# Kernel optimization log

Hardware: AMD Instinct MI355X
Metric: run time of the kernel (lower is better)

Reference implementation:

```python
import jax, jax.numpy as jnp
import numpy as np

B, T, S, E, H, L, V = 32, 64, 64, 512, 1024, 2, 32000


def setup_inputs() -> dict:
    key = jax.random.key(0)
    ks = jax.random.split(key, 20)
    std = 0.02
    inp = {
        "x": jax.random.randint(ks[0], (B, T), 0, V),
        "h0": jax.random.normal(ks[1], (L, B, H), jnp.float32) * std,
        "c0": jax.random.normal(ks[2], (L, B, H), jnp.float32) * std,
        "x_enc": jax.random.normal(ks[3], (B, S, H), jnp.float32),
        "emb": jax.random.normal(ks[4], (V, E), jnp.float32) * std,
        # layer 0: input = concat(emb, prev_out) -> E + H
        "Wih0": jax.random.normal(ks[5], (4 * H, E + H), jnp.float32) * std,
        "Whh0": jax.random.normal(ks[6], (4 * H, H), jnp.float32) * std,
        "bih0": jnp.zeros((4 * H,), jnp.float32),
        "bhh0": jnp.zeros((4 * H,), jnp.float32),
        # layer 1: input = h of layer 0 -> H
        "Wih1": jax.random.normal(ks[7], (4 * H, H), jnp.float32) * std,
        "Whh1": jax.random.normal(ks[8], (4 * H, H), jnp.float32) * std,
        "bih1": jnp.zeros((4 * H,), jnp.float32),
        "bhh1": jnp.zeros((4 * H,), jnp.float32),
        # attention linear H->H
        "Wa": jax.random.normal(ks[9], (H, H), jnp.float32) * std,
        "ba": jnp.zeros((H,), jnp.float32),
        # output linear 2H->H
        "Wl": jax.random.normal(ks[10], (H, 2 * H), jnp.float32) * std,
        "bl": jnp.zeros((H,), jnp.float32),
        # generator H->V
        "Wg": jax.random.normal(ks[11], (V, H), jnp.float32) * std,
        "bg": jnp.zeros((V,), jnp.float32),
    }
    return inp


def _decoder_fwd(x, h0, c0, x_enc, emb, Wih0, Whh0, bih0, bhh0,
                 Wih1, Whh1, bih1, bhh1, Wa, ba, Wl, bl, Wg, bg):
    layers = ((Wih0, Whh0, bih0, bhh0), (Wih1, Whh1, bih1, bhh1))
    xs = emb[x]  # [B, T, E]

    def lstm_cell(inp, h_prev, c_prev, Wih, Whh, bih, bhh):
        g = inp @ Wih.T + bih + h_prev @ Whh.T + bhh  # [B, 4H]
        i_, f_, g_, o_ = jnp.split(g, 4, axis=-1)     # torch order: i,f,g,o
        c_new = jax.nn.sigmoid(f_) * c_prev + jax.nn.sigmoid(i_) * jnp.tanh(g_)
        h_new = jax.nn.sigmoid(o_) * jnp.tanh(c_new)
        return h_new, c_new

    def step(carry, e_t):
        h, c, prev = carry  # h,c: [L,B,H]; prev: [B,H]
        inp = jnp.concatenate([e_t, prev], axis=-1)  # [B, E+H]
        hs, cs = [], []
        for l, (Wih, Whh, bih, bhh) in enumerate(layers):
            h_new, c_new = lstm_cell(inp, h[l], c[l], Wih, Whh, bih, bhh)
            hs.append(h_new); cs.append(c_new)
            inp = h_new
        z = inp  # top-layer hidden [B, H]
        # attention: score = linear(z) . x_enc^T
        s = jnp.einsum('bh,bsh->bs', z @ Wa.T + ba, x_enc)  # [B, S]
        w = jax.nn.softmax(s, axis=-1)
        ctx = jnp.einsum('bs,bsh->bh', w, x_enc)            # [B, H]
        out = jnp.tanh(jnp.concatenate([z, ctx], axis=-1) @ Wl.T + bl)  # [B, H]
        return (jnp.stack(hs), jnp.stack(cs), out), out

    prev0 = jnp.zeros((x.shape[0], Wl.shape[0]), xs.dtype)
    e_seq = jnp.swapaxes(xs[:, :-1, :], 0, 1)  # [T-1, B, E]
    _, outs = jax.lax.scan(step, (h0, c0, prev0), e_seq)
    outs = jnp.swapaxes(outs, 0, 1)  # [B, T-1, H]
    # dropout p=0.0 (eval) -> identity; generator: linear + log_softmax
    return jax.nn.log_softmax(outs @ Wg.T + bg, axis=-1)  # [B, T-1, V]


def reference(x, h0, c0, x_enc, emb, Wih0, Whh0, bih0, bhh0,
              Wih1, Whh1, bih1, bhh1, Wa, ba, Wl, bl, Wg, bg):
    return _decoder_fwd(x, h0, c0, x_enc, emb, Wih0, Whh0, bih0, bhh0,
                        Wih1, Whh1, bih1, bhh1, Wa, ba, Wl, bl, Wg, bg)
```

## Files before the change

kernel.cpp:

```cpp
#include <hip/hip_runtime.h>
#include <math.h>

#define BB 32
#define HH 1024
#define EE 512
#define TT 63
#define SS 64
#define VV 32000

__global__ __launch_bounds__(256)
void init_kernel(const float* __restrict__ h0, const float* __restrict__ c0,
                 float* __restrict__ h_state, float* __restrict__ c_state,
                 float* __restrict__ prev0)
{
    int i = blockIdx.x * 256 + threadIdx.x;
    if (i < 2 * BB * HH) { h_state[i] = h0[i]; c_state[i] = c0[i]; }
    if (i < BB * HH) prev0[i] = 0.f;
}

__global__ __launch_bounds__(128)
void embed_kernel(const int* __restrict__ x, const float* __restrict__ emb,
                  float* __restrict__ xs)
{
    int t = blockIdx.x >> 5;
    int b = blockIdx.x & 31;
    int tok = x[b * 64 + t];
    const float4* src = (const float4*)(emb + (size_t)tok * EE);
    float4* dst = (float4*)(xs + ((size_t)t * BB + b) * EE);
    dst[threadIdx.x] = src[threadIdx.x];
}

__global__ __launch_bounds__(256)
void lstm_step_kernel(const float* __restrict__ src0, int K0,
                      const float* __restrict__ src1, int K1,
                      const float* __restrict__ Wih, const float* __restrict__ Whh,
                      const float* __restrict__ bih, const float* __restrict__ bhh,
                      const float* __restrict__ h_prev, const float* __restrict__ c_prev,
                      float* __restrict__ h_new, float* __restrict__ c_new)
{
    __shared__ float lds[64 * 33];
    const int tid  = threadIdx.x;
    const int b    = tid & 31;
    const int hl   = tid >> 5;
    const int h    = blockIdx.x * 8 + hl;
    const int lane = tid & 63;
    const int wv   = tid >> 6;
    const int KW   = K0 + K1;
    const int Ktot = KW + HH;

    float acc0 = 0.f, acc1 = 0.f, acc2 = 0.f, acc3 = 0.f;

    for (int k0 = 0; k0 < Ktot; k0 += 64) {
        const float* s; int koff; int stride;
        if (k0 < K0)      { s = src0;   koff = k0;        stride = K0; }
        else if (k0 < KW) { s = src1;   koff = k0 - K0;   stride = K1; }
        else              { s = h_prev; koff = k0 - KW;   stride = HH; }
        #pragma unroll
        for (int r = 0; r < 8; ++r) {
            int bb = wv * 8 + r;
            lds[lane * 33 + bb] = s[(size_t)bb * stride + koff + lane];
        }
        __syncthreads();

        const float *wi, *wf, *wg, *wo;
        if (k0 < KW) {
            wi = Wih + (size_t)h            * KW + k0;
            wf = Wih + (size_t)(HH   + h)   * KW + k0;
            wg = Wih + (size_t)(2*HH + h)   * KW + k0;
            wo = Wih + (size_t)(3*HH + h)   * KW + k0;
        } else {
            int c = k0 - KW;
            wi = Whh + (size_t)h            * HH + c;
            wf = Whh + (size_t)(HH   + h)   * HH + c;
            wg = Whh + (size_t)(2*HH + h)   * HH + c;
            wo = Whh + (size_t)(3*HH + h)   * HH + c;
        }
        #pragma unroll
        for (int k = 0; k < 64; k += 4) {
            float4 vi = *(const float4*)(wi + k);
            float4 vf = *(const float4*)(wf + k);
            float4 vg = *(const float4*)(wg + k);
            float4 vo = *(const float4*)(wo + k);
            float x0 = lds[(k+0)*33 + b];
            float x1 = lds[(k+1)*33 + b];
            float x2 = lds[(k+2)*33 + b];
            float x3 = lds[(k+3)*33 + b];
            acc0 = fmaf(x0, vi.x, acc0); acc0 = fmaf(x1, vi.y, acc0);
            acc0 = fmaf(x2, vi.z, acc0); acc0 = fmaf(x3, vi.w, acc0);
            acc1 = fmaf(x0, vf.x, acc1); acc1 = fmaf(x1, vf.y, acc1);
            acc1 = fmaf(x2, vf.z, acc1); acc1 = fmaf(x3, vf.w, acc1);
            acc2 = fmaf(x0, vg.x, acc2); acc2 = fmaf(x1, vg.y, acc2);
            acc2 = fmaf(x2, vg.z, acc2); acc2 = fmaf(x3, vg.w, acc2);
            acc3 = fmaf(x0, vo.x, acc3); acc3 = fmaf(x1, vo.y, acc3);
            acc3 = fmaf(x2, vo.z, acc3); acc3 = fmaf(x3, vo.w, acc3);
        }
        __syncthreads();
    }

    float gi = acc0 + bih[h]        + bhh[h];
    float gf = acc1 + bih[HH + h]   + bhh[HH + h];
    float gg = acc2 + bih[2*HH + h] + bhh[2*HH + h];
    float go = acc3 + bih[3*HH + h] + bhh[3*HH + h];
    float si = 1.f / (1.f + expf(-gi));
    float sf = 1.f / (1.f + expf(-gf));
    float so = 1.f / (1.f + expf(-go));
    float cp = c_prev[(size_t)b * HH + h];
    float cn = sf * cp + si * tanhf(gg);
    float hn = so * tanhf(cn);
    h_new[(size_t)b * HH + h] = hn;
    c_new[(size_t)b * HH + h] = cn;
}

__global__ __launch_bounds__(256)
void linear_kernel(const float* __restrict__ src0, int K0,
                   const float* __restrict__ src1, int K1,
                   const float* __restrict__ W, const float* __restrict__ bias,
                   float* __restrict__ out, int N, int act)
{
    __shared__ float lds[64 * 33];
    const int tid  = threadIdx.x;
    const int b    = tid & 31;
    const int nl   = tid >> 5;
    const int n    = blockIdx.x * 8 + nl;
    const int lane = tid & 63;
    const int wv   = tid >> 6;
    const int K    = K0 + K1;
    float acc = 0.f;
    const float* wr = W + (size_t)n * K;
    for (int k0 = 0; k0 < K; k0 += 64) {
        const float* s; int koff; int stride;
        if (k0 < K0) { s = src0; koff = k0;      stride = K0; }
        else         { s = src1; koff = k0 - K0; stride = K1; }
        #pragma unroll
        for (int r = 0; r < 8; ++r) {
            int bb = wv * 8 + r;
            lds[lane * 33 + bb] = s[(size_t)bb * stride + koff + lane];
        }
        __syncthreads();
        #pragma unroll
        for (int k = 0; k < 64; k += 4) {
            float4 w4 = *(const float4*)(wr + k0 + k);
            acc = fmaf(lds[(k+0)*33 + b], w4.x, acc);
            acc = fmaf(lds[(k+1)*33 + b], w4.y, acc);
            acc = fmaf(lds[(k+2)*33 + b], w4.z, acc);
            acc = fmaf(lds[(k+3)*33 + b], w4.w, acc);
        }
        __syncthreads();
    }
    float r = acc + bias[n];
    if (act) r = tanhf(r);
    out[(size_t)b * N + n] = r;
}

__global__ __launch_bounds__(256)
void attn_kernel(const float* __restrict__ za, const float* __restrict__ x_enc,
                 float* __restrict__ ctx)
{
    __shared__ float zs[HH];
    __shared__ float pp[256];
    __shared__ float wgt[SS];
    const int tid = threadIdx.x;
    const int b = blockIdx.x;
    for (int i = tid; i < HH; i += 256) zs[i] = za[(size_t)b * HH + i];
    __syncthreads();
    int j = tid >> 2, part = tid & 3;
    const float* xe = x_enc + ((size_t)b * SS + j) * HH + part * 256;
    const float* zp = zs + part * 256;
    float p = 0.f;
    for (int k = 0; k < 256; ++k) p = fmaf(zp[k], xe[k], p);
    pp[tid] = p;
    __syncthreads();
    if (tid < SS) {
        float sc = pp[tid*4] + pp[tid*4+1] + pp[tid*4+2] + pp[tid*4+3];
        float m = sc;
        for (int off = 32; off; off >>= 1) m = fmaxf(m, __shfl_xor(m, off));
        float e = expf(sc - m);
        float ssum = e;
        for (int off = 32; off; off >>= 1) ssum += __shfl_xor(ssum, off);
        wgt[tid] = e / ssum;
    }
    __syncthreads();
    for (int k = tid; k < HH; k += 256) {
        float a = 0.f;
        const float* xb = x_enc + (size_t)b * SS * HH + k;
        #pragma unroll 8
        for (int jj = 0; jj < SS; ++jj) a = fmaf(wgt[jj], xb[(size_t)jj * HH], a);
        ctx[(size_t)b * HH + k] = a;
    }
}

__global__ __launch_bounds__(256)
void gen_gemm_kernel(const float* __restrict__ outs, const float* __restrict__ Wg,
                     const float* __restrict__ bg, float* __restrict__ out)
{
    __shared__ float As[32 * 68];
    __shared__ float Bs[64 * 68];
    const int tid = threadIdx.x;
    const int tn = tid & 15, tm = tid >> 4;
    const int vbase = blockIdx.x * 64;
    const int rbase = blockIdx.y * 32;
    float acc[2][4] = {};

    const int arow = tid >> 3;
    const int acol = (tid & 7) * 8;
    int rg = rbase + arow;
    int ab = rg / TT, at = rg % TT;
    const float* asrc = outs + ((size_t)at * BB + ab) * HH + acol;
    const int brow = tid >> 2;
    const int bcol = (tid & 3) * 16;
    const float* bsrc = Wg + (size_t)(vbase + brow) * HH + bcol;

    for (int k0 = 0; k0 < HH; k0 += 64) {
        float4 a4a = *(const float4*)(asrc + k0);
        float4 a4b = *(const float4*)(asrc + k0 + 4);
        *(float4*)&As[arow*68 + acol]     = a4a;
        *(float4*)&As[arow*68 + acol + 4] = a4b;
        float4 q0 = *(const float4*)(bsrc + k0);
        float4 q1 = *(const float4*)(bsrc + k0 + 4);
        float4 q2 = *(const float4*)(bsrc + k0 + 8);
        float4 q3 = *(const float4*)(bsrc + k0 + 12);
        *(float4*)&Bs[brow*68 + bcol]      = q0;
        *(float4*)&Bs[brow*68 + bcol + 4]  = q1;
        *(float4*)&Bs[brow*68 + bcol + 8]  = q2;
        *(float4*)&Bs[brow*68 + bcol + 12] = q3;
        __syncthreads();
        #pragma unroll
        for (int k = 0; k < 64; k += 4) {
            float4 a0 = *(const float4*)&As[(tm*2+0)*68 + k];
            float4 a1 = *(const float4*)&As[(tm*2+1)*68 + k];
            float4 b0 = *(const float4*)&Bs[(tn*4+0)*68 + k];
            float4 b1 = *(const float4*)&Bs[(tn*4+1)*68 + k];
            float4 b2 = *(const float4*)&Bs[(tn*4+2)*68 + k];
            float4 b3 = *(const float4*)&Bs[(tn*4+3)*68 + k];
            acc[0][0] += a0.x*b0.x + a0.y*b0.y + a0.z*b0.z + a0.w*b0.w;
            acc[0][1] += a0.x*b1.x + a0.y*b1.y + a0.z*b1.z + a0.w*b1.w;
            acc[0][2] += a0.x*b2.x + a0.y*b2.y + a0.z*b2.z + a0.w*b2.w;
            acc[0][3] += a0.x*b3.x + a0.y*b3.y + a0.z*b3.z + a0.w*b3.w;
            acc[1][0] += a1.x*b0.x + a1.y*b0.y + a1.z*b0.z + a1.w*b0.w;
            acc[1][1] += a1.x*b1.x + a1.y*b1.y + a1.z*b1.z + a1.w*b1.w;
            acc[1][2] += a1.x*b2.x + a1.y*b2.y + a1.z*b2.z + a1.w*b2.w;
            acc[1][3] += a1.x*b3.x + a1.y*b3.y + a1.z*b3.z + a1.w*b3.w;
        }
        __syncthreads();
    }
    #pragma unroll
    for (int i = 0; i < 2; ++i) {
        int r = rbase + tm*2 + i;
        #pragma unroll
        for (int jj = 0; jj < 4; ++jj) {
            int v = vbase + tn*4 + jj;
            out[(size_t)r * VV + v] = acc[i][jj] + bg[v];
        }
    }
}

__global__ __launch_bounds__(256)
void logsoftmax_kernel(float* __restrict__ out)
{
    __shared__ float red[4];
    __shared__ float red2[4];
    const int tid = threadIdx.x;
    float* row = out + (size_t)blockIdx.x * VV;
    float m = -1e30f;
    for (int i = tid; i < VV; i += 256) m = fmaxf(m, row[i]);
    for (int off = 32; off; off >>= 1) m = fmaxf(m, __shfl_xor(m, off));
    if ((tid & 63) == 0) red[tid >> 6] = m;
    __syncthreads();
    m = fmaxf(fmaxf(red[0], red[1]), fmaxf(red[2], red[3]));
    float s = 0.f;
    for (int i = tid; i < VV; i += 256) s += expf(row[i] - m);
    for (int off = 32; off; off >>= 1) s += __shfl_xor(s, off);
    if ((tid & 63) == 0) red2[tid >> 6] = s;
    __syncthreads();
    s = red2[0] + red2[1] + red2[2] + red2[3];
    float lse = m + logf(s);
    for (int i = tid; i < VV; i += 256) row[i] = row[i] - lse;
}

extern "C" void kernel_launch(void* const* d_in, const int* in_sizes, int n_in,
                              void* d_out, int out_size, void* d_ws, size_t ws_size,
                              hipStream_t stream)
{
    (void)in_sizes; (void)n_in; (void)out_size; (void)ws_size;
    const int*   x    = (const int*)  d_in[0];
    const float* h0   = (const float*)d_in[1];
    const float* c0   = (const float*)d_in[2];
    const float* x_enc= (const float*)d_in[3];
    const float* emb  = (const float*)d_in[4];
    const float* Wih0 = (const float*)d_in[5];
    const float* Whh0 = (const float*)d_in[6];
    const float* bih0 = (const float*)d_in[7];
    const float* bhh0 = (const float*)d_in[8];
    const float* Wih1 = (const float*)d_in[9];
    const float* Whh1 = (const float*)d_in[10];
    const float* bih1 = (const float*)d_in[11];
    const float* bhh1 = (const float*)d_in[12];
    const float* Wa   = (const float*)d_in[13];
    const float* ba   = (const float*)d_in[14];
    const float* Wl   = (const float*)d_in[15];
    const float* bl   = (const float*)d_in[16];
    const float* Wg   = (const float*)d_in[17];
    const float* bg   = (const float*)d_in[18];
    float* out = (float*)d_out;

    float* ws      = (float*)d_ws;
    float* h_state = ws;
    float* c_state = h_state + 131072;
    float* prev0   = c_state + 131072;
    float* za      = prev0   + 32768;
    float* ctx     = za      + 32768;
    float* xs      = ctx     + 32768;
    float* outs    = xs      + (size_t)TT * BB * EE;

    init_kernel<<<256, 256, 0, stream>>>(h0, c0, h_state, c_state, prev0);
    embed_kernel<<<TT * BB, 128, 0, stream>>>(x, emb, xs);

    for (int t = 0; t < TT; ++t) {
        const float* e_t  = xs + (size_t)t * BB * EE;
        const float* prev = (t == 0) ? prev0 : (outs + (size_t)(t - 1) * BB * HH);
        float* hc = h_state + (size_t)(t & 1) * 65536;
        float* hn = h_state + (size_t)((t + 1) & 1) * 65536;
        float* cc = c_state + (size_t)(t & 1) * 65536;
        float* cn = c_state + (size_t)((t + 1) & 1) * 65536;
        lstm_step_kernel<<<128, 256, 0, stream>>>(e_t, EE, prev, HH,
            Wih0, Whh0, bih0, bhh0, hc, cc, hn, cn);
        lstm_step_kernel<<<128, 256, 0, stream>>>(hn, HH, nullptr, 0,
            Wih1, Whh1, bih1, bhh1, hc + 32768, cc + 32768, hn + 32768, cn + 32768);
        linear_kernel<<<128, 256, 0, stream>>>(hn + 32768, HH, nullptr, 0,
            Wa, ba, za, HH, 0);
        attn_kernel<<<BB, 256, 0, stream>>>(za, x_enc, ctx);
        linear_kernel<<<128, 256, 0, stream>>>(hn + 32768, HH, ctx, HH,
            Wl, bl, outs + (size_t)t * BB * HH, HH, 1);
    }

    gen_gemm_kernel<<<dim3(VV / 64, 2016 / 32), 256, 0, stream>>>(outs, Wg, bg, out);
    logsoftmax_kernel<<<2016, 256, 0, stream>>>(out);
}
```

Measured before the change: 28.03 ms.

## Run decoder loop as persistent cooperative kernel with transposed weights and split-K GEMMs

Replaces the per-timestep launches with one cooperative persistent kernel that steps through all timesteps using grid-wide syncs. Weights are pre-transposed into the output buffer used as scratch, and the gate GEMMs are split over K into partial sums that a finalize phase reduces. The attention projection is moved off the recurrence by precomputing Wa applied to x_enc plus a bias term. The aim is to remove launch overhead and raise parallelism in the small-batch GEMVs, at the cost of grid-sync latency, extra partial-sum traffic and reliance on cooperative-launch support.

```diff
diff --git a/kernel.cpp b/kernel.cpp
--- a/kernel.cpp
+++ b/kernel.cpp
@@ -1,5 +1,8 @@
 #include <hip/hip_runtime.h>
+#include <hip/hip_cooperative_groups.h>
 #include <math.h>
+
+namespace cg = cooperative_groups;
 
 #define BB 32
 #define HH 1024
@@ -8,185 +11,316 @@
 #define SS 64
 #define VV 32000
 
-__global__ __launch_bounds__(256)
-void init_kernel(const float* __restrict__ h0, const float* __restrict__ c0,
-                 float* __restrict__ h_state, float* __restrict__ c_state,
-                 float* __restrict__ prev0)
+static const size_t OWT0 = 0;
+static const size_t OWT1 = 10485760;
+static const size_t OWLT = 18874368;
+static const size_t OXC0 = 20971520;
+static const size_t OXC1 = 26214400;
+static const size_t OGP  = 30408704;
+static const size_t OOP  = 34603008;
+static const size_t OPE  = 35651584;
+static const size_t OCB  = 37748736;
+
+__device__ __forceinline__ void fma4(float4& a, float s, const float4 w) {
+    a.x = fmaf(s, w.x, a.x);
+    a.y = fmaf(s, w.y, a.y);
+    a.z = fmaf(s, w.z, a.z);
+    a.w = fmaf(s, w.w, a.w);
+}
+
+template<int WPITCH, int NRT>
+__device__ __forceinline__ void pgemm(const float* __restrict__ W,
+                                      const float* __restrict__ X, int xpitch,
+                                      int kslice, float* __restrict__ P)
+{
+    const int tid = threadIdx.x, lane = tid & 63, wv = tid >> 6;
+    const int nU = NRT * 32;
+    for (int u = blockIdx.x; u < nU; u += gridDim.x) {
+        const int rt = u >> 5, kg = u & 31;
+        const int r0 = rt * 256 + lane * 4;
+        const int b0 = wv * 8;
+        const int kbase = kg * kslice;
+        const float* wb = W + (size_t)kbase * WPITCH + r0;
+        const float* xb = X + (size_t)b0 * xpitch + kbase;
+        float4 acc[8];
+        #pragma unroll
+        for (int i = 0; i < 8; ++i) acc[i] = make_float4(0.f, 0.f, 0.f, 0.f);
+        #pragma unroll 2
+        for (int kk = 0; kk < kslice; kk += 4) {
+            float4 w0 = *(const float4*)(wb + (size_t)(kk + 0) * WPITCH);
+            float4 w1 = *(const float4*)(wb + (size_t)(kk + 1) * WPITCH);
+            float4 w2 = *(const float4*)(wb + (size_t)(kk + 2) * WPITCH);
+            float4 w3 = *(const float4*)(wb + (size_t)(kk + 3) * WPITCH);
+            #pragma unroll
+            for (int i = 0; i < 8; ++i) {
+                float4 xv = *(const float4*)(xb + (size_t)i * xpitch + kk);
+                fma4(acc[i], xv.x, w0);
+                fma4(acc[i], xv.y, w1);
+                fma4(acc[i], xv.z, w2);
+                fma4(acc[i], xv.w, w3);
+            }
+        }
+        float* pp = P + ((size_t)kg * BB + b0) * WPITCH + r0;
+        #pragma unroll
+        for (int i = 0; i < 8; ++i) *(float4*)(pp + (size_t)i * WPITCH) = acc[i];
+    }
+}
+
+__device__ __forceinline__ void lstm_fin(const float* __restrict__ P,
+    const float* __restrict__ bih, const float* __restrict__ bhh,
+    float* __restrict__ cst,
+    float* __restrict__ hA, int pA, int oA,
+    float* __restrict__ hB, int pB, int oB,
+    float* __restrict__ smem)
+{
+    const int tid = threadIdx.x, lane = tid & 63, g = tid >> 6;
+    for (int u = blockIdx.x; u < 512; u += gridDim.x) {
+        const int b = u >> 4, hc = u & 15;
+        const int h = hc * 64 + lane;
+        float s = 0.f;
+        #pragma unroll
+        for (int sl = 0; sl < 32; ++sl)
+            s += P[((size_t)sl * BB + b) * 4096 + g * 1024 + h];
+        s += bih[g * 1024 + h] + bhh[g * 1024 + h];
+        smem[g * 64 + lane] = s;
+        __syncthreads();
+        if (tid < 64) {
+            float gi = smem[lane], gf = smem[64 + lane];
+            float gg = smem[128 + lane], go = smem[192 + lane];
+            float si = 1.f / (1.f + expf(-gi));
+            float sf = 1.f / (1.f + expf(-gf));
+            float so = 1.f / (1.f + expf(-go));
+            float cp = cst[(size_t)b * 1024 + h];
+            float cn = sf * cp + si * tanhf(gg);
+            float hn = so * tanhf(cn);
+            cst[(size_t)b * 1024 + h] = cn;
+            hA[(size_t)b * pA + oA + h] = hn;
+            hB[(size_t)b * pB + oB + h] = hn;
+        }
+        __syncthreads();
+    }
+}
+
+__device__ __forceinline__ void attn_phase(const float* __restrict__ xenc,
+    const float* __restrict__ pe, const float* __restrict__ cb,
+    float* __restrict__ zc, float* __restrict__ smem)
+{
+    const int tid = threadIdx.x;
+    float* zl = smem;
+    float* pp = smem + 1024;
+    float* wt = smem + 1280;
+    for (int u = blockIdx.x; u < 32; u += gridDim.x) {
+        const int b = u;
+        for (int i = tid; i < 1024; i += 256) zl[i] = zc[(size_t)b * 2048 + i];
+        __syncthreads();
+        {
+            const int j = tid >> 2, part = tid & 3;
+            const float* per = pe + ((size_t)b * 64 + j) * 1024 + part * 256;
+            const float* zp = zl + part * 256;
+            float p0 = 0.f, p1 = 0.f, p2 = 0.f, p3 = 0.f;
+            for (int k = 0; k < 256; k += 4) {
+                p0 = fmaf(zp[k], per[k], p0);
+                p1 = fmaf(zp[k + 1], per[k + 1], p1);
+                p2 = fmaf(zp[k + 2], per[k + 2], p2);
+                p3 = fmaf(zp[k + 3], per[k + 3], p3);
+            }
+            pp[tid] = (p0 + p1) + (p2 + p3);
+        }
+        __syncthreads();
+        if (tid < 64) {
+            float sc = pp[tid * 4] + pp[tid * 4 + 1] + pp[tid * 4 + 2] + pp[tid * 4 + 3]
+                     + cb[b * 64 + tid];
+            float m = sc;
+            #pragma unroll
+            for (int off = 32; off; off >>= 1) m = fmaxf(m, __shfl_xor(m, off));
+            float e = expf(sc - m);
+            float ss = e;
+            #pragma unroll
+            for (int off = 32; off; off >>= 1) ss += __shfl_xor(ss, off);
+            wt[tid] = e / ss;
+        }
+        __syncthreads();
+        for (int k = tid; k < 1024; k += 256) {
+            float a = 0.f;
+            const float* xe = xenc + (size_t)b * (SS * HH) + k;
+            #pragma unroll 8
+            for (int j = 0; j < SS; ++j) a = fmaf(wt[j], xe[(size_t)j * HH], a);
+            zc[(size_t)b * 2048 + 1024 + k] = a;
+        }
+        __syncthreads();
+    }
+}
+
+__device__ __forceinline__ void out_fin(const float* __restrict__ P,
+    const float* __restrict__ bl, float* __restrict__ outs_t,
+    float* __restrict__ xc0n, float* __restrict__ smem)
+{
+    const int tid = threadIdx.x, lane = tid & 63, wv = tid >> 6;
+    for (int u = blockIdx.x; u < 512; u += gridDim.x) {
+        const int b = u >> 4, nc = u & 15;
+        const int n = nc * 64 + lane;
+        float s = 0.f;
+        #pragma unroll
+        for (int q = 0; q < 8; ++q)
+            s += P[((size_t)(wv * 8 + q) * BB + b) * 1024 + n];
+        smem[wv * 64 + lane] = s;
+        __syncthreads();
+        if (tid < 64) {
+            float tot = smem[lane] + smem[64 + lane] + smem[128 + lane]
+                      + smem[192 + lane] + bl[n];
+            float r = tanhf(tot);
+            outs_t[(size_t)b * 1024 + n] = r;
+            xc0n[(size_t)b * 2560 + 512 + n] = r;
+        }
+        __syncthreads();
+    }
+}
+
+__global__ __launch_bounds__(256, 2)
+void decoder_loop(const float* __restrict__ xenc,
+                  const float* __restrict__ bih0, const float* __restrict__ bhh0,
+                  const float* __restrict__ bih1, const float* __restrict__ bhh1,
+                  const float* __restrict__ bl,
+                  float* __restrict__ scratch,
+                  float* __restrict__ c_state, float* __restrict__ zc,
+                  float* __restrict__ outs)
+{
+    __shared__ float smem[1344];
+    cg::grid_group grid = cg::this_grid();
+    const float* WT0 = scratch + OWT0;
+    const float* WT1 = scratch + OWT1;
+    const float* WlT = scratch + OWLT;
+    float* xcat0 = scratch + OXC0;
+    float* xcat1 = scratch + OXC1;
+    float* gatesP = scratch + OGP;
+    float* outP = scratch + OOP;
+    const float* pe = scratch + OPE;
+    const float* cb = scratch + OCB;
+
+    for (int t = 0; t < TT; ++t) {
+        float* xc0t = xcat0 + (size_t)t * BB * 2560;
+        float* xc0n = xcat0 + (size_t)(t + 1) * BB * 2560;
+        float* xc1t = xcat1 + (size_t)t * BB * 2048;
+        float* xc1n = xcat1 + (size_t)(t + 1) * BB * 2048;
+
+        pgemm<4096, 16>(WT0, xc0t, 2560, 80, gatesP);
+        grid.sync();
+        lstm_fin(gatesP, bih0, bhh0, c_state,
+                 xc1t, 2048, 0, xc0n, 2560, 1536, smem);
+        grid.sync();
+        pgemm<4096, 16>(WT1, xc1t, 2048, 64, gatesP);
+        grid.sync();
+        lstm_fin(gatesP, bih1, bhh1, c_state + 32768,
+                 zc, 2048, 0, xc1n, 2048, 1024, smem);
+        grid.sync();
+        attn_phase(xenc, pe, cb, zc, smem);
+        grid.sync();
+        pgemm<1024, 4>(WlT, zc, 2048, 64, outP);
+        grid.sync();
+        out_fin(outP, bl, outs + (size_t)t * BB * HH, xc0n, smem);
+        grid.sync();
+    }
+}
+
+__global__ __launch_bounds__(256, 2)
+void k_gate_gemm(const float* __restrict__ W, const float* __restrict__ X,
+                 int xpitch, int kslice, float* __restrict__ P)
+{ pgemm<4096, 16>(W, X, xpitch, kslice, P); }
+
+__global__ __launch_bounds__(256, 2)
+void k_out_gemm(const float* __restrict__ W, const float* __restrict__ X,
+                float* __restrict__ P)
+{ pgemm<1024, 4>(W, X, 2048, 64, P); }
+
+__global__ __launch_bounds__(256)
+void k_lstm_fin(const float* __restrict__ P, const float* __restrict__ bih,
+                const float* __restrict__ bhh, float* __restrict__ cst,
+                float* __restrict__ hA, int pA, int oA,
+                float* __restrict__ hB, int pB, int oB)
+{ __shared__ float smem[256]; lstm_fin(P, bih, bhh, cst, hA, pA, oA, hB, pB, oB, smem); }
+
+__global__ __launch_bounds__(256)
+void k_attn(const float* __restrict__ xenc, const float* __restrict__ pe,
+            const float* __restrict__ cb, float* __restrict__ zc)
+{ __shared__ float smem[1344]; attn_phase(xenc, pe, cb, zc, smem); }
+
+__global__ __launch_bounds__(256)
+void k_out_fin(const float* __restrict__ P, const float* __restrict__ bl,
+               float* __restrict__ outs_t, float* __restrict__ xc0n)
+{ __shared__ float smem[256]; out_fin(P, bl, outs_t, xc0n, smem); }
+
+__global__ __launch_bounds__(256)
+void init_kernel2(const float* __restrict__ h0, const float* __restrict__ c0,
+                  float* __restrict__ c_state, float* __restrict__ xcat0,
+                  float* __restrict__ xcat1)
 {
     int i = blockIdx.x * 256 + threadIdx.x;
-    if (i < 2 * BB * HH) { h_state[i] = h0[i]; c_state[i] = c0[i]; }
-    if (i < BB * HH) prev0[i] = 0.f;
+    c_state[i] = c0[i];
+    int b = (i >> 10) & 31, h = i & 1023, l = i >> 15;
+    if (l == 0) {
+        xcat0[(size_t)b * 2560 + 1536 + h] = h0[i];
+        xcat0[(size_t)b * 2560 + 512 + h] = 0.f;
+    } else {
+        xcat1[(size_t)b * 2048 + 1024 + h] = h0[i];
+    }
 }
 
 __global__ __launch_bounds__(128)
-void embed_kernel(const int* __restrict__ x, const float* __restrict__ emb,
-                  float* __restrict__ xs)
-{
-    int t = blockIdx.x >> 5;
-    int b = blockIdx.x & 31;
+void embed_kernel2(const int* __restrict__ x, const float* __restrict__ emb,
+                   float* __restrict__ xcat0)
+{
+    int t = blockIdx.x >> 5, b = blockIdx.x & 31;
     int tok = x[b * 64 + t];
     const float4* src = (const float4*)(emb + (size_t)tok * EE);
-    float4* dst = (float4*)(xs + ((size_t)t * BB + b) * EE);
+    float4* dst = (float4*)(xcat0 + ((size_t)t * BB + b) * 2560);
     dst[threadIdx.x] = src[threadIdx.x];
 }
 
 __global__ __launch_bounds__(256)
-void lstm_step_kernel(const float* __restrict__ src0, int K0,
-                      const float* __restrict__ src1, int K1,
-                      const float* __restrict__ Wih, const float* __restrict__ Whh,
-                      const float* __restrict__ bih, const float* __restrict__ bhh,
-                      const float* __restrict__ h_prev, const float* __restrict__ c_prev,
-                      float* __restrict__ h_new, float* __restrict__ c_new)
-{
-    __shared__ float lds[64 * 33];
-    const int tid  = threadIdx.x;
-    const int b    = tid & 31;
-    const int hl   = tid >> 5;
-    const int h    = blockIdx.x * 8 + hl;
-    const int lane = tid & 63;
-    const int wv   = tid >> 6;
-    const int KW   = K0 + K1;
-    const int Ktot = KW + HH;
-
-    float acc0 = 0.f, acc1 = 0.f, acc2 = 0.f, acc3 = 0.f;
-
-    for (int k0 = 0; k0 < Ktot; k0 += 64) {
-        const float* s; int koff; int stride;
-        if (k0 < K0)      { s = src0;   koff = k0;        stride = K0; }
-        else if (k0 < KW) { s = src1;   koff = k0 - K0;   stride = K1; }
-        else              { s = h_prev; koff = k0 - KW;   stride = HH; }
-        #pragma unroll
-        for (int r = 0; r < 8; ++r) {
-            int bb = wv * 8 + r;
-            lds[lane * 33 + bb] = s[(size_t)bb * stride + koff + lane];
-        }
-        __syncthreads();
-
-        const float *wi, *wf, *wg, *wo;
-        if (k0 < KW) {
-            wi = Wih + (size_t)h            * KW + k0;
-            wf = Wih + (size_t)(HH   + h)   * KW + k0;
-            wg = Wih + (size_t)(2*HH + h)   * KW + k0;
-            wo = Wih + (size_t)(3*HH + h)   * KW + k0;
-        } else {
-            int c = k0 - KW;
-            wi = Whh + (size_t)h            * HH + c;
-            wf = Whh + (size_t)(HH   + h)   * HH + c;
-            wg = Whh + (size_t)(2*HH + h)   * HH + c;
-            wo = Whh + (size_t)(3*HH + h)   * HH + c;
-        }
-        #pragma unroll
-        for (int k = 0; k < 64; k += 4) {
-            float4 vi = *(const float4*)(wi + k);
-            float4 vf = *(const float4*)(wf + k);
-            float4 vg = *(const float4*)(wg + k);
-            float4 vo = *(const float4*)(wo + k);
-            float x0 = lds[(k+0)*33 + b];
-            float x1 = lds[(k+1)*33 + b];
-            float x2 = lds[(k+2)*33 + b];
-            float x3 = lds[(k+3)*33 + b];
-            acc0 = fmaf(x0, vi.x, acc0); acc0 = fmaf(x1, vi.y, acc0);
-            acc0 = fmaf(x2, vi.z, acc0); acc0 = fmaf(x3, vi.w, acc0);
-            acc1 = fmaf(x0, vf.x, acc1); acc1 = fmaf(x1, vf.y, acc1);
-            acc1 = fmaf(x2, vf.z, acc1); acc1 = fmaf(x3, vf.w, acc1);
-            acc2 = fmaf(x0, vg.x, acc2); acc2 = fmaf(x1, vg.y, acc2);
-            acc2 = fmaf(x2, vg.z, acc2); acc2 = fmaf(x3, vg.w, acc2);
-            acc3 = fmaf(x0, vo.x, acc3); acc3 = fmaf(x1, vo.y, acc3);
-            acc3 = fmaf(x2, vo.z, acc3); acc3 = fmaf(x3, vo.w, acc3);
-        }
-        __syncthreads();
-    }
-
-    float gi = acc0 + bih[h]        + bhh[h];
-    float gf = acc1 + bih[HH + h]   + bhh[HH + h];
-    float gg = acc2 + bih[2*HH + h] + bhh[2*HH + h];
-    float go = acc3 + bih[3*HH + h] + bhh[3*HH + h];
-    float si = 1.f / (1.f + expf(-gi));
-    float sf = 1.f / (1.f + expf(-gf));
-    float so = 1.f / (1.f + expf(-go));
-    float cp = c_prev[(size_t)b * HH + h];
-    float cn = sf * cp + si * tanhf(gg);
-    float hn = so * tanhf(cn);
-    h_new[(size_t)b * HH + h] = hn;
-    c_new[(size_t)b * HH + h] = cn;
-}
-
-__global__ __launch_bounds__(256)
-void linear_kernel(const float* __restrict__ src0, int K0,
-                   const float* __restrict__ src1, int K1,
-                   const float* __restrict__ W, const float* __restrict__ bias,
-                   float* __restrict__ out, int N, int act)
-{
-    __shared__ float lds[64 * 33];
-    const int tid  = threadIdx.x;
-    const int b    = tid & 31;
-    const int nl   = tid >> 5;
-    const int n    = blockIdx.x * 8 + nl;
-    const int lane = tid & 63;
-    const int wv   = tid >> 6;
-    const int K    = K0 + K1;
-    float acc = 0.f;
-    const float* wr = W + (size_t)n * K;
-    for (int k0 = 0; k0 < K; k0 += 64) {
-        const float* s; int koff; int stride;
-        if (k0 < K0) { s = src0; koff = k0;      stride = K0; }
-        else         { s = src1; koff = k0 - K0; stride = K1; }
-        #pragma unroll
-        for (int r = 0; r < 8; ++r) {
-            int bb = wv * 8 + r;
-            lds[lane * 33 + bb] = s[(size_t)bb * stride + koff + lane];
-        }
-        __syncthreads();
-        #pragma unroll
-        for (int k = 0; k < 64; k += 4) {
-            float4 w4 = *(const float4*)(wr + k0 + k);
-            acc = fmaf(lds[(k+0)*33 + b], w4.x, acc);
-            acc = fmaf(lds[(k+1)*33 + b], w4.y, acc);
-            acc = fmaf(lds[(k+2)*33 + b], w4.z, acc);
-            acc = fmaf(lds[(k+3)*33 + b], w4.w, acc);
-        }
-        __syncthreads();
-    }
-    float r = acc + bias[n];
-    if (act) r = tanhf(r);
-    out[(size_t)b * N + n] = r;
-}
-
-__global__ __launch_bounds__(256)
-void attn_kernel(const float* __restrict__ za, const float* __restrict__ x_enc,
-                 float* __restrict__ ctx)
-{
-    __shared__ float zs[HH];
-    __shared__ float pp[256];
-    __shared__ float wgt[SS];
-    const int tid = threadIdx.x;
-    const int b = blockIdx.x;
-    for (int i = tid; i < HH; i += 256) zs[i] = za[(size_t)b * HH + i];
+void transpose_kernel(const float* __restrict__ src, int C,
+                      float* __restrict__ dst, int dpitch)
+{
+    __shared__ float tile[32][33];
+    const int tx = threadIdx.x & 31, ty = threadIdx.x >> 5;
+    const int c0 = blockIdx.x * 32, r0 = blockIdx.y * 32;
+    #pragma unroll
+    for (int i = 0; i < 32; i += 8)
+        tile[ty + i][tx] = src[(size_t)(r0 + ty + i) * C + (c0 + tx)];
     __syncthreads();
-    int j = tid >> 2, part = tid & 3;
-    const float* xe = x_enc + ((size_t)b * SS + j) * HH + part * 256;
-    const float* zp = zs + part * 256;
-    float p = 0.f;
-    for (int k = 0; k < 256; ++k) p = fmaf(zp[k], xe[k], p);
-    pp[tid] = p;
-    __syncthreads();
-    if (tid < SS) {
-        float sc = pp[tid*4] + pp[tid*4+1] + pp[tid*4+2] + pp[tid*4+3];
-        float m = sc;
-        for (int off = 32; off; off >>= 1) m = fmaxf(m, __shfl_xor(m, off));
-        float e = expf(sc - m);
-        float ssum = e;
-        for (int off = 32; off; off >>= 1) ssum += __shfl_xor(ssum, off);
-        wgt[tid] = e / ssum;
-    }
-    __syncthreads();
-    for (int k = tid; k < HH; k += 256) {
-        float a = 0.f;
-        const float* xb = x_enc + (size_t)b * SS * HH + k;
-        #pragma unroll 8
-        for (int jj = 0; jj < SS; ++jj) a = fmaf(wgt[jj], xb[(size_t)jj * HH], a);
-        ctx[(size_t)b * HH + k] = a;
-    }
+    #pragma unroll
+    for (int i = 0; i < 32; i += 8)
+        dst[(size_t)(c0 + ty + i) * dpitch + (r0 + tx)] = tile[tx][ty + i];
+}
+
+__global__ __launch_bounds__(256)
+void projenc_kernel(const float* __restrict__ xenc, const float* __restrict__ Wa,
+                    float* __restrict__ pe)
+{
+    const int r = blockIdx.x;
+    const int n0 = threadIdx.x * 4;
+    const float* xe = xenc + (size_t)r * HH;
+    float4 a = make_float4(0.f, 0.f, 0.f, 0.f);
+    for (int h = 0; h < HH; h += 4) {
+        float4 xv = *(const float4*)(xe + h);
+        fma4(a, xv.x, *(const float4*)(Wa + (size_t)h * HH + n0));
+        fma4(a, xv.y, *(const float4*)(Wa + (size_t)(h + 1) * HH + n0));
+        fma4(a, xv.z, *(const float4*)(Wa + (size_t)(h + 2) * HH + n0));
+        fma4(a, xv.w, *(const float4*)(Wa + (size_t)(h + 3) * HH + n0));
+    }
+    *(float4*)(pe + (size_t)r * HH + n0) = a;
+}
+
+__global__ __launch_bounds__(64)
+void cbias_kernel(const float* __restrict__ xenc, const float* __restrict__ ba,
+                  float* __restrict__ cb)
+{
+    const int r = blockIdx.x;
+    const float* xe = xenc + (size_t)r * HH;
+    float s = 0.f;
+    for (int k = threadIdx.x; k < HH; k += 64) s = fmaf(ba[k], xe[k], s);
+    #pragma unroll
+    for (int off = 32; off; off >>= 1) s += __shfl_xor(s, off);
+    if (threadIdx.x == 0) cb[r] = s;
 }
 
 __global__ __launch_bounds__(256)
@@ -213,42 +347,42 @@
     for (int k0 = 0; k0 < HH; k0 += 64) {
         float4 a4a = *(const float4*)(asrc + k0);
         float4 a4b = *(const float4*)(asrc + k0 + 4);
-        *(float4*)&As[arow*68 + acol]     = a4a;
-        *(float4*)&As[arow*68 + acol + 4] = a4b;
+        *(float4*)&As[arow * 68 + acol] = a4a;
+        *(float4*)&As[arow * 68 + acol + 4] = a4b;
         float4 q0 = *(const float4*)(bsrc + k0);
         float4 q1 = *(const float4*)(bsrc + k0 + 4);
         float4 q2 = *(const float4*)(bsrc + k0 + 8);
         float4 q3 = *(const float4*)(bsrc + k0 + 12);
-        *(float4*)&Bs[brow*68 + bcol]      = q0;
-        *(float4*)&Bs[brow*68 + bcol + 4]  = q1;
-        *(float4*)&Bs[brow*68 + bcol + 8]  = q2;
-        *(float4*)&Bs[brow*68 + bcol + 12] = q3;
+        *(float4*)&Bs[brow * 68 + bcol] = q0;
+        *(float4*)&Bs[brow * 68 + bcol + 4] = q1;
+        *(float4*)&Bs[brow * 68 + bcol + 8] = q2;
+        *(float4*)&Bs[brow * 68 + bcol + 12] = q3;
         __syncthreads();
         #pragma unroll
         for (int k = 0; k < 64; k += 4) {
-            float4 a0 = *(const float4*)&As[(tm*2+0)*68 + k];
-            float4 a1 = *(const float4*)&As[(tm*2+1)*68 + k];
-            float4 b0 = *(const float4*)&Bs[(tn*4+0)*68 + k];
-            float4 b1 = *(const float4*)&Bs[(tn*4+1)*68 + k];
-            float4 b2 = *(const float4*)&Bs[(tn*4+2)*68 + k];
-            float4 b3 = *(const float4*)&Bs[(tn*4+3)*68 + k];
-            acc[0][0] += a0.x*b0.x + a0.y*b0.y + a0.z*b0.z + a0.w*b0.w;
-            acc[0][1] += a0.x*b1.x + a0.y*b1.y + a0.z*b1.z + a0.w*b1.w;
-            acc[0][2] += a0.x*b2.x + a0.y*b2.y + a0.z*b2.z + a0.w*b2.w;
-            acc[0][3] += a0.x*b3.x + a0.y*b3.y + a0.z*b3.z + a0.w*b3.w;
-            acc[1][0] += a1.x*b0.x + a1.y*b0.y + a1.z*b0.z + a1.w*b0.w;
-            acc[1][1] += a1.x*b1.x + a1.y*b1.y + a1.z*b1.z + a1.w*b1.w;
-            acc[1][2] += a1.x*b2.x + a1.y*b2.y + a1.z*b2.z + a1.w*b2.w;
-            acc[1][3] += a1.x*b3.x + a1.y*b3.y + a1.z*b3.z + a1.w*b3.w;
+            float4 a0 = *(const float4*)&As[(tm * 2 + 0) * 68 + k];
+            float4 a1 = *(const float4*)&As[(tm * 2 + 1) * 68 + k];
+            float4 b0 = *(const float4*)&Bs[(tn * 4 + 0) * 68 + k];
+            float4 b1 = *(const float4*)&Bs[(tn * 4 + 1) * 68 + k];
+            float4 b2 = *(const float4*)&Bs[(tn * 4 + 2) * 68 + k];
+            float4 b3 = *(const float4*)&Bs[(tn * 4 + 3) * 68 + k];
+            acc[0][0] += a0.x * b0.x + a0.y * b0.y + a0.z * b0.z + a0.w * b0.w;
+            acc[0][1] += a0.x * b1.x + a0.y * b1.y + a0.z * b1.z + a0.w * b1.w;
+            acc[0][2] += a0.x * b2.x + a0.y * b2.y + a0.z * b2.z + a0.w * b2.w;
+            acc[0][3] += a0.x * b3.x + a0.y * b3.y + a0.z * b3.z + a0.w * b3.w;
+            acc[1][0] += a1.x * b0.x + a1.y * b0.y + a1.z * b0.z + a1.w * b0.w;
+            acc[1][1] += a1.x * b1.x + a1.y * b1.y + a1.z * b1.z + a1.w * b1.w;
+            acc[1][2] += a1.x * b2.x + a1.y * b2.y + a1.z * b2.z + a1.w * b2.w;
+            acc[1][3] += a1.x * b3.x + a1.y * b3.y + a1.z * b3.z + a1.w * b3.w;
         }
         __syncthreads();
     }
     #pragma unroll
     for (int i = 0; i < 2; ++i) {
-        int r = rbase + tm*2 + i;
+        int r = rbase + tm * 2 + i;
         #pragma unroll
         for (int jj = 0; jj < 4; ++jj) {
-            int v = vbase + tn*4 + jj;
+            int v = vbase + tn * 4 + jj;
             out[(size_t)r * VV + v] = acc[i][jj] + bg[v];
         }
     }
@@ -302,35 +436,73 @@
     const float* Wg   = (const float*)d_in[17];
     const float* bg   = (const float*)d_in[18];
     float* out = (float*)d_out;
+    float* scratch = (float*)d_out;
 
     float* ws      = (float*)d_ws;
-    float* h_state = ws;
-    float* c_state = h_state + 131072;
-    float* prev0   = c_state + 131072;
-    float* za      = prev0   + 32768;
-    float* ctx     = za      + 32768;
-    float* xs      = ctx     + 32768;
-    float* outs    = xs      + (size_t)TT * BB * EE;
-
-    init_kernel<<<256, 256, 0, stream>>>(h0, c0, h_state, c_state, prev0);
-    embed_kernel<<<TT * BB, 128, 0, stream>>>(x, emb, xs);
-
-    for (int t = 0; t < TT; ++t) {
-        const float* e_t  = xs + (size_t)t * BB * EE;
-        const float* prev = (t == 0) ? prev0 : (outs + (size_t)(t - 1) * BB * HH);
-        float* hc = h_state + (size_t)(t & 1) * 65536;
-        float* hn = h_state + (size_t)((t + 1) & 1) * 65536;
-        float* cc = c_state + (size_t)(t & 1) * 65536;
-        float* cn = c_state + (size_t)((t + 1) & 1) * 65536;
-        lstm_step_kernel<<<128, 256, 0, stream>>>(e_t, EE, prev, HH,
-            Wih0, Whh0, bih0, bhh0, hc, cc, hn, cn);
-        lstm_step_kernel<<<128, 256, 0, stream>>>(hn, HH, nullptr, 0,
-            Wih1, Whh1, bih1, bhh1, hc + 32768, cc + 32768, hn + 32768, cn + 32768);
-        linear_kernel<<<128, 256, 0, stream>>>(hn + 32768, HH, nullptr, 0,
-            Wa, ba, za, HH, 0);
-        attn_kernel<<<BB, 256, 0, stream>>>(za, x_enc, ctx);
-        linear_kernel<<<128, 256, 0, stream>>>(hn + 32768, HH, ctx, HH,
-            Wl, bl, outs + (size_t)t * BB * HH, HH, 1);
+    float* c_state = ws;
+    float* zc      = ws + 65536;
+    float* outs    = ws + 131072;
+
+    init_kernel2<<<256, 256, 0, stream>>>(h0, c0, c_state,
+                                          scratch + OXC0, scratch + OXC1);
+    embed_kernel2<<<TT * BB, 128, 0, stream>>>(x, emb, scratch + OXC0);
+    transpose_kernel<<<dim3(48, 128), 256, 0, stream>>>(Wih0, 1536, scratch + OWT0, 4096);
+    transpose_kernel<<<dim3(32, 128), 256, 0, stream>>>(Whh0, 1024,
+                         scratch + OWT0 + (size_t)1536 * 4096, 4096);
+    transpose_kernel<<<dim3(32, 128), 256, 0, stream>>>(Wih1, 1024, scratch + OWT1, 4096);
+    transpose_kernel<<<dim3(32, 128), 256, 0, stream>>>(Whh1, 1024,
+                         scratch + OWT1 + (size_t)1024 * 4096, 4096);
+    transpose_kernel<<<dim3(64, 32), 256, 0, stream>>>(Wl, 2048, scratch + OWLT, 1024);
+    projenc_kernel<<<2048, 256, 0, stream>>>(x_enc, Wa, scratch + OPE);
+    cbias_kernel<<<2048, 64, 0, stream>>>(x_enc, ba, scratch + OCB);
+
+    static int coopGrid = -2;
+    if (coopGrid == -2) {
+        int dev = 0; hipGetDevice(&dev);
+        int coop = 0;
+        hipDeviceGetAttribute(&coop, hipDeviceAttributeCooperativeLaunch, dev);
+        if (!coop) coopGrid = 0;
+        else {
+            int occ = 0;
+            if (hipOccupancyMaxActiveBlocksPerMultiprocessor(&occ, decoder_loop,
+                    256, 0) != hipSuccess || occ < 1) occ = 0;
+            int nCU = 256;
+            hipDeviceProp_t prop;
+            if (hipGetDeviceProperties(&prop, dev) == hipSuccess && prop.multiProcessorCount > 0)
+                nCU = prop.multiProcessorCount;
+            int g = occ * nCU;
+            if (g > 512) g = 512;
+            coopGrid = g;
+        }
+    }
+
+    bool done = false;
+    if (coopGrid > 0) {
+        void* args[] = {(void*)&x_enc, (void*)&bih0, (void*)&bhh0, (void*)&bih1,
+                        (void*)&bhh1, (void*)&bl, (void*)&scratch, (void*)&c_state,
+                        (void*)&zc, (void*)&outs};
+        hipError_t e = hipLaunchCooperativeKernel(decoder_loop, dim3(coopGrid),
+                                                  dim3(256), args, 0u, stream);
+        if (e == hipSuccess) done = true;
+        else coopGrid = 0;
+    }
+    if (!done) {
+        for (int t = 0; t < TT; ++t) {
+            float* xc0t = scratch + OXC0 + (size_t)t * BB * 2560;
+            float* xc0n = scratch + OXC0 + (size_t)(t + 1) * BB * 2560;
+            float* xc1t = scratch + OXC1 + (size_t)t * BB * 2048;
+            float* xc1n = scratch + OXC1 + (size_t)(t + 1) * BB * 2048;
+            k_gate_gemm<<<512, 256, 0, stream>>>(scratch + OWT0, xc0t, 2560, 80, scratch + OGP);
+            k_lstm_fin<<<512, 256, 0, stream>>>(scratch + OGP, bih0, bhh0, c_state,
+                                                xc1t, 2048, 0, xc0n, 2560, 1536);
+            k_gate_gemm<<<512, 256, 0, stream>>>(scratch + OWT1, xc1t, 2048, 64, scratch + OGP);
+            k_lstm_fin<<<512, 256, 0, stream>>>(scratch + OGP, bih1, bhh1, c_state + 32768,
+                                                zc, 2048, 0, xc1n, 2048, 1024);
+            k_attn<<<32, 256, 0, stream>>>(x_enc, scratch + OPE, scratch + OCB, zc);
+            k_out_gemm<<<128, 256, 0, stream>>>(scratch + OWLT, zc, scratch + OOP);
+            k_out_fin<<<512, 256, 0, stream>>>(scratch + OOP, bl,
+                                               outs + (size_t)t * BB * HH, xc0n);
+        }
     }
 
     gen_gemm_kernel<<<dim3(VV / 64, 2016 / 32), 256, 0, stream>>>(outs, Wg, bg, out);
```

New measurement: 24.13 ms. 1.16x faster.
